# Kernel optimization log

Measured on AMD Instinct MI355X. Metric: run time of the kernel, lower is better.

## Reference

```python
import jax, jax.numpy as jnp
import numpy as np

N = 100000


def _gcn_norm(edge_index, edge_weight, n):
    # PyG gcn_norm: add self loops (weight 1), symmetric normalization.
    src = jnp.concatenate([edge_index[0], jnp.arange(n, dtype=edge_index.dtype)])
    dst = jnp.concatenate([edge_index[1], jnp.arange(n, dtype=edge_index.dtype)])
    ew = jnp.concatenate([edge_weight, jnp.ones((n,), edge_weight.dtype)])
    deg = jax.ops.segment_sum(ew, dst, num_segments=n)  # [N]
    dis = jnp.where(deg > 0, deg ** -0.5, 0.0).astype(edge_weight.dtype)
    norm = dis[src] * ew * dis[dst]  # [E+N]
    return src, dst, norm


def _gcn_conv(x, src, dst, norm, W, b, n):
    h = x @ W                                   # [N, out]
    msg = h[src] * norm[:, None]                # [E+N, out] gather + scale
    out = jax.ops.segment_sum(msg, dst, num_segments=n)  # scatter-add
    return out + b


def setup_inputs() -> dict:
    key = jax.random.key(0)
    ks = jax.random.split(key, 8)
    E = 1600000
    F_in, H, C = 256, 64, 40
    return {
        "x": jax.random.normal(ks[0], (N, F_in), jnp.float32),
        "edge_index": jax.random.randint(ks[1], (2, E), 0, N, jnp.int32),
        "edge_weight": jax.random.uniform(ks[2], (E,), jnp.float32),
        "W0": jax.random.normal(ks[3], (F_in, H), jnp.float32) / np.sqrt(F_in),
        "b0": jnp.zeros((H,), jnp.float32),
        "W1": jax.random.normal(ks[4], (H, H), jnp.float32) / np.sqrt(H),
        "b1": jnp.zeros((H,), jnp.float32),
        "W2": jax.random.normal(ks[5], (H, C), jnp.float32) / np.sqrt(H),
        "b2": jnp.zeros((C,), jnp.float32),
    }


def reference(x, edge_index, edge_weight, W0, b0, W1, b1, W2, b2):
    n = x.shape[0]
    # Edge structure is identical across layers -> compute norm once.
    src, dst, norm = _gcn_norm(edge_index, edge_weight, n)
    # num_layers=3: two hidden GCN layers with relu (dropout = identity in eval)
    h = jax.nn.relu(_gcn_conv(x, src, dst, norm, W0, b0, n))
    h = jax.nn.relu(_gcn_conv(h, src, dst, norm, W1, b1, n))
    h = _gcn_conv(h, src, dst, norm, W2, b2, n)
    return jax.nn.log_softmax(h, axis=1)
```

## Files before the change

### kernel.cpp

```cpp
#include <hip/hip_runtime.h>
#include <math.h>


__device__ __forceinline__ unsigned short f2bf(float f) {
    unsigned u = __float_as_uint(f);
    u += 0x7FFFu + ((u >> 16) & 1u);
    return (unsigned short)(u >> 16);
}
__device__ __forceinline__ float bf2f(unsigned short h) {
    return __uint_as_float(((unsigned)h) << 16);
}

__global__ void k_scan1(const int* __restrict__ cnt, int* __restrict__ excl,
                        int* __restrict__ bsum, int n) {
    __shared__ int sm[256];
    int tid = threadIdx.x;
    int i = blockIdx.x * 256 + tid;
    int v = (i < n) ? cnt[i] : 0;
    sm[tid] = v;
    __syncthreads();
    for (int off = 1; off < 256; off <<= 1) {
        int t = (tid >= off) ? sm[tid - off] : 0;
        __syncthreads();
        sm[tid] += t;
        __syncthreads();
    }
    if (i < n) excl[i] = sm[tid] - v;
    if (tid == 255) bsum[blockIdx.x] = sm[255];
}

__global__ void k_scan2(const int* __restrict__ bsum, int* __restrict__ boff, int nb) {
    __shared__ int sm[512];
    int tid = threadIdx.x;
    int v = (tid < nb) ? bsum[tid] : 0;
    sm[tid] = v;
    __syncthreads();
    for (int off = 1; off < 512; off <<= 1) {
        int t = (tid >= off) ? sm[tid - off] : 0;
        __syncthreads();
        sm[tid] += t;
        __syncthreads();
    }
    boff[tid] = sm[tid] - v;
}

__global__ void k_scan3(int* __restrict__ rowptr, const int* __restrict__ boff,
                        int n, int E) {
    int i = blockIdx.x * blockDim.x + threadIdx.x;
    if (i < n) rowptr[i] += boff[i >> 8];
    if (i == 0) rowptr[n] = E;
}

__global__ void k_place(const int* __restrict__ src, const int* __restrict__ dst,
                        const float* __restrict__ ew, const int* __restrict__ rowptr,
                        const int* __restrict__ pos, unsigned long long* __restrict__ pairP,
                        int E) {
    int e = blockIdx.x * blockDim.x + threadIdx.x;
    if (e < E) {
        int d = dst[e];
        int p = rowptr[d] + pos[e];
        unsigned long long pk = (unsigned long long)__float_as_uint(ew[e]) << 32
                              | (unsigned int)src[e];
        pairP[p] = pk;
    }
}

__global__ void k_deg_dis(const unsigned long long* __restrict__ pairP,
                          const int* __restrict__ rowptr, float* __restrict__ dis, int n) {
    int i = blockIdx.x * blockDim.x + threadIdx.x;
    if (i >= n) return;
    int a = rowptr[i], b = rowptr[i + 1];
    float s = 1.0f;
    for (int p = a; p < b; ++p)
        s += __uint_as_float((unsigned int)(pairP[p] >> 32));
    dis[i] = (s > 0.f) ? rsqrtf(s) : 0.f;
}

__global__ void k_norm_csr(unsigned long long* __restrict__ pairP,
                           const int* __restrict__ rowptr,
                           const float* __restrict__ dis, int n) {
    int i = blockIdx.x * blockDim.x + threadIdx.x;
    if (i >= n) return;
    int a = rowptr[i], b = rowptr[i + 1];
    float dd = dis[i];
    for (int p = a; p < b; ++p) {
        unsigned long long pk = pairP[p];
        int s = (int)(unsigned int)pk;
        float w = __uint_as_float((unsigned int)(pk >> 32));
        float nrm = dis[s] * w * dd;
        pairP[p] = ((unsigned long long)__float_as_uint(nrm) << 32) | (unsigned int)s;
    }
}

template<int K, int NOUT, bool RELU_IN>
__device__ __forceinline__ void gemm_tile_body(
    const float* __restrict__ X, const float* __restrict__ W,
    unsigned short* __restrict__ HB, int nrows, int tile)
{
    constexpr int BM = 64, BN = 64, BK = 32;
    constexpr int T  = K / BK;
    __shared__ float As[BK][BM + 4];
    __shared__ float Bs[BK][BN + 4];

    const int tid = (int)threadIdx.x;
    const int tx  = tid & 15;
    const int ty  = tid >> 4;
    const int r0  = tile * BM;

    const int ar = tid >> 3;
    const int aq = tid & 7;
    const int bk = tid >> 4;
    const int bc = tid & 15;

    const int rowA0 = min(r0 + ar,      nrows - 1);
    const int rowA1 = min(r0 + ar + 32, nrows - 1);
    const float* pA0 = X + (size_t)rowA0 * K + aq * 4;
    const float* pA1 = X + (size_t)rowA1 * K + aq * 4;
    const bool wok = (bc * 4 + 3 < NOUT);
    const float* pB0 = W + (size_t)bk * NOUT + bc * 4;
    const float* pB1 = W + (size_t)(bk + 16) * NOUT + bc * 4;
    const float4 z4 = make_float4(0.f, 0.f, 0.f, 0.f);

    float4 ra0, ra1, rb0, rb1;
    ra0 = *(const float4*)pA0;
    ra1 = *(const float4*)pA1;
    rb0 = wok ? *(const float4*)pB0 : z4;
    rb1 = wok ? *(const float4*)pB1 : z4;

    float acc[4][4] = {};

#pragma unroll 1
    for (int t = 0; t < T; ++t) {
        if (RELU_IN) {
            ra0.x = fmaxf(ra0.x, 0.f); ra0.y = fmaxf(ra0.y, 0.f);
            ra0.z = fmaxf(ra0.z, 0.f); ra0.w = fmaxf(ra0.w, 0.f);
            ra1.x = fmaxf(ra1.x, 0.f); ra1.y = fmaxf(ra1.y, 0.f);
            ra1.z = fmaxf(ra1.z, 0.f); ra1.w = fmaxf(ra1.w, 0.f);
        }
        As[aq * 4 + 0][ar]      = ra0.x;
        As[aq * 4 + 1][ar]      = ra0.y;
        As[aq * 4 + 2][ar]      = ra0.z;
        As[aq * 4 + 3][ar]      = ra0.w;
        As[aq * 4 + 0][ar + 32] = ra1.x;
        As[aq * 4 + 1][ar + 32] = ra1.y;
        As[aq * 4 + 2][ar + 32] = ra1.z;
        As[aq * 4 + 3][ar + 32] = ra1.w;
        *(float4*)&Bs[bk][bc * 4]      = rb0;
        *(float4*)&Bs[bk + 16][bc * 4] = rb1;
        __syncthreads();

        if (t + 1 < T) {
            const int ko = (t + 1) * BK;
            ra0 = *(const float4*)(pA0 + ko);
            ra1 = *(const float4*)(pA1 + ko);
            rb0 = wok ? *(const float4*)(pB0 + (size_t)ko * NOUT) : z4;
            rb1 = wok ? *(const float4*)(pB1 + (size_t)ko * NOUT) : z4;
        }

#pragma unroll
        for (int kk = 0; kk < BK; ++kk) {
            float4 a = *(const float4*)&As[kk][ty * 4];
            float4 b = *(const float4*)&Bs[kk][tx * 4];
            acc[0][0] += a.x * b.x; acc[0][1] += a.x * b.y; acc[0][2] += a.x * b.z; acc[0][3] += a.x * b.w;
            acc[1][0] += a.y * b.x; acc[1][1] += a.y * b.y; acc[1][2] += a.y * b.z; acc[1][3] += a.y * b.w;
            acc[2][0] += a.z * b.x; acc[2][1] += a.z * b.y; acc[2][2] += a.z * b.z; acc[2][3] += a.z * b.w;
            acc[3][0] += a.w * b.x; acc[3][1] += a.w * b.y; acc[3][2] += a.w * b.z; acc[3][3] += a.w * b.w;
        }
        __syncthreads();
    }

    if (tx * 4 + 3 < NOUT) {
#pragma unroll
        for (int i = 0; i < 4; ++i) {
            int row = r0 + ty * 4 + i;
            if (row < nrows) {
                ushort4 hv;
                hv.x = f2bf(acc[i][0]); hv.y = f2bf(acc[i][1]);
                hv.z = f2bf(acc[i][2]); hv.w = f2bf(acc[i][3]);
                *(ushort4*)&HB[(size_t)row * NOUT + tx * 4] = hv;
            }
        }
    }
}

template<int K, int NOUT, bool RELU_IN>
__global__ __launch_bounds__(256) void k_gemm(
    const float* __restrict__ X, const float* __restrict__ W,
    unsigned short* __restrict__ HB, int nrows)
{
    gemm_tile_body<K, NOUT, RELU_IN>(X, W, HB, nrows, (int)blockIdx.x);
}

template<int K, int NOUT, bool RELU_IN>
__global__ __launch_bounds__(256) void k_gemm_cnt(
    const float* __restrict__ X, const float* __restrict__ W,
    unsigned short* __restrict__ HB, int nrows, int ntiles, int ncnt,
    const int* __restrict__ dst, int* __restrict__ cnt, int* __restrict__ pos, int E)
{
    const int b  = (int)blockIdx.x;
    const int m  = min(ntiles, ncnt);
    bool isCnt; int idx;
    if (b < 2 * m) {
        isCnt = ((b & 1) == 0);
        idx   = b >> 1;
    } else {
        int rem = b - 2 * m;
        isCnt = (ncnt > ntiles);
        idx   = m + rem;
    }
    if (!isCnt) {
        gemm_tile_body<K, NOUT, RELU_IN>(X, W, HB, nrows, idx);
    } else {
        int e0     = idx * 256 + (int)threadIdx.x;
        int stride = ncnt * 256;
        for (int e = e0; e < E; e += stride)
            pos[e] = atomicAdd(&cnt[dst[e]], 1);
    }
}

template<int F, bool LSM>
__global__ __launch_bounds__(256) void k_node_agg(
    const unsigned short* __restrict__ hB, const float* __restrict__ dis,
    const float* __restrict__ bias, const int* __restrict__ rowptr,
    const unsigned long long* __restrict__ pairP,
    float* __restrict__ out, int n)
{
    const int lane = threadIdx.x & 63;
    int row = (int)((blockIdx.x * blockDim.x + threadIdx.x) >> 6);
    if (row >= n) return;
    row = __builtin_amdgcn_readfirstlane(row);

    const int a = rowptr[row], b = rowptr[row + 1];
    float d  = dis[row];
    float dd = d * d;
    float sum = 0.f;
    if (lane < F) sum = bf2f(hB[(size_t)row * F + lane]) * dd + bias[lane];

    int j = a;
    for (; j + 4 <= b; j += 4) {
        unsigned long long p0 = pairP[j],     p1 = pairP[j + 1];
        unsigned long long p2 = pairP[j + 2], p3 = pairP[j + 3];
        int   s0 = (int)(unsigned int)p0, s1 = (int)(unsigned int)p1;
        int   s2 = (int)(unsigned int)p2, s3 = (int)(unsigned int)p3;
        float w0 = __uint_as_float((unsigned int)(p0 >> 32));
        float w1 = __uint_as_float((unsigned int)(p1 >> 32));
        float w2 = __uint_as_float((unsigned int)(p2 >> 32));
        float w3 = __uint_as_float((unsigned int)(p3 >> 32));
        if (lane < F) {
            sum += bf2f(hB[(size_t)s0 * F + lane]) * w0;
            sum += bf2f(hB[(size_t)s1 * F + lane]) * w1;
            sum += bf2f(hB[(size_t)s2 * F + lane]) * w2;
            sum += bf2f(hB[(size_t)s3 * F + lane]) * w3;
        }
    }
    for (; j < b; ++j) {
        unsigned long long p = pairP[j];
        int s = (int)(unsigned int)p;
        float w = __uint_as_float((unsigned int)(p >> 32));
        if (lane < F) sum += bf2f(hB[(size_t)s * F + lane]) * w;
    }

    if (LSM) {
        float v = (lane < F) ? sum : -INFINITY;
        float m = v;
#pragma unroll
        for (int off = 32; off; off >>= 1) m = fmaxf(m, __shfl_xor(m, off));
        float e = (lane < F) ? expf(v - m) : 0.f;
        float s2 = e;
#pragma unroll
        for (int off = 32; off; off >>= 1) s2 += __shfl_xor(s2, off);
        float ls = logf(s2);
        if (lane < F) out[(size_t)row * F + lane] = v - m - ls;
    } else {
        if (lane < F) out[(size_t)row * F + lane] = sum;
    }
}

extern "C" void kernel_launch(void* const* d_in, const int* in_sizes, int n_in,
                              void* d_out, int out_size, void* d_ws, size_t ws_size,
                              hipStream_t stream) {
    const float* x  = (const float*)d_in[0];
    const int*   ei = (const int*)  d_in[1];
    const float* ew = (const float*)d_in[2];
    const float* W0 = (const float*)d_in[3];
    const float* b0 = (const float*)d_in[4];
    const float* W1 = (const float*)d_in[5];
    const float* b1 = (const float*)d_in[6];
    const float* W2 = (const float*)d_in[7];
    const float* b2 = (const float*)d_in[8];

    const int E   = in_sizes[2];
    const int H   = in_sizes[4];
    const int Fin = in_sizes[3] / H;
    const int N   = in_sizes[0] / Fin;
    (void)n_in; (void)out_size; (void)ws_size;

    const int* srcv = ei;
    const int* dstv = ei + E;

    float* ws = (float*)d_ws;
    size_t o = 0;
    auto alloc = [&](size_t cnt_) { size_t p = o; o += (cnt_ + 63) & ~(size_t)63; return p; };
    float* dis   = ws + alloc(N);
    float* bufB  = ws + alloc((size_t)N * 64);
    unsigned short* hB = (unsigned short*)(ws + alloc((size_t)N * 32));
    unsigned long long* pairP = (unsigned long long*)(ws + alloc((size_t)E * 2));
    int*   rowptr= (int*)(ws + alloc(N + 1));
    int*   cnt   = (int*)(ws + alloc(N));
    int*   pos   = (int*)(ws + alloc(E));
    int*   bsum  = (int*)(ws + alloc(512));
    int*   boff  = (int*)(ws + alloc(512));
    float* outf  = (float*)d_out;

    const int TB  = 256;
    const int nb1 = (N + 255) / 256;
    const int ntiles = (N + 63) / 64;
    const int XB  = 1024;

    (void)hipMemsetAsync(cnt, 0, (size_t)N * sizeof(int), stream);
    {
        const int m = (ntiles < XB) ? ntiles : XB;
        const int grid = 2 * m + ((ntiles > XB) ? (ntiles - XB) : (XB - ntiles));
        k_gemm_cnt<256, 64, false><<<grid, TB, 0, stream>>>(
            x, W0, hB, N, ntiles, XB, dstv, cnt, pos, E);
    }

    k_scan1<<<nb1, 256, 0, stream>>>(cnt, rowptr, bsum, N);
    k_scan2<<<1, 512, 0, stream>>>(bsum, boff, nb1);
    k_scan3<<<(N + TB - 1) / TB, TB, 0, stream>>>(rowptr, boff, N, E);

    k_place<<<(E + TB - 1) / TB, TB, 0, stream>>>(srcv, dstv, ew, rowptr, pos, pairP, E);

    k_deg_dis <<<(N + TB - 1) / TB, TB, 0, stream>>>(pairP, rowptr, dis, N);
    k_norm_csr<<<(N + TB - 1) / TB, TB, 0, stream>>>(pairP, rowptr, dis, N);

    const int aggGrid = (N * 64 + TB - 1) / TB;

    k_node_agg<64, false><<<aggGrid, TB, 0, stream>>>(hB, dis, b0, rowptr, pairP, bufB, N);

    k_gemm<64, 64, true><<<ntiles, TB, 0, stream>>>(bufB, W1, hB, N);
    k_node_agg<64, false><<<aggGrid, TB, 0, stream>>>(hB, dis, b1, rowptr, pairP, bufB, N);

    k_gemm<64, 40, true><<<ntiles, TB, 0, stream>>>(bufB, W2, hB, N);
    k_node_agg<40, true><<<aggGrid, TB, 0, stream>>>(hB, dis, b2, rowptr, pairP, outf, N);
}
```

Measured before the change: 342.5 us.

## Use wavefront-per-row for degree/norm kernels and stage edge pairs in LDS

The degree and normalization kernels switch from one thread per row to one 64-lane wavefront per row, reading each row's edges with coalesced strided loads and reducing with shuffles. The aggregation kernel now loads up to 64 packed (src, weight) pairs per row cooperatively into shared memory and reads them from LDS, instead of every lane issuing the same global loads. The goal is to cut uncoalesced serial edge walks and redundant global traffic. In exchange, short rows (about 16 edges on average) leave most lanes idle, and the degree sum is added in a different order.

```diff
diff --git a/kernel.cpp b/kernel.cpp
--- a/kernel.cpp
+++ b/kernel.cpp
@@ -65,30 +65,42 @@
     }
 }
 
-__global__ void k_deg_dis(const unsigned long long* __restrict__ pairP,
-                          const int* __restrict__ rowptr, float* __restrict__ dis, int n) {
-    int i = blockIdx.x * blockDim.x + threadIdx.x;
-    if (i >= n) return;
-    int a = rowptr[i], b = rowptr[i + 1];
-    float s = 1.0f;
-    for (int p = a; p < b; ++p)
-        s += __uint_as_float((unsigned int)(pairP[p] >> 32));
-    dis[i] = (s > 0.f) ? rsqrtf(s) : 0.f;
-}
-
-__global__ void k_norm_csr(unsigned long long* __restrict__ pairP,
-                           const int* __restrict__ rowptr,
-                           const float* __restrict__ dis, int n) {
-    int i = blockIdx.x * blockDim.x + threadIdx.x;
-    if (i >= n) return;
-    int a = rowptr[i], b = rowptr[i + 1];
-    float dd = dis[i];
-    for (int p = a; p < b; ++p) {
-        unsigned long long pk = pairP[p];
+__global__ __launch_bounds__(256) void k_deg_dis(
+    const unsigned long long* __restrict__ pairP,
+    const int* __restrict__ rowptr, float* __restrict__ dis, int n)
+{
+    const int lane = threadIdx.x & 63;
+    int row = (int)((blockIdx.x * blockDim.x + threadIdx.x) >> 6);
+    if (row >= n) return;
+    row = __builtin_amdgcn_readfirstlane(row);
+    const int a = rowptr[row], b = rowptr[row + 1];
+    float s = 0.f;
+    for (int idx = a + lane; idx < b; idx += 64)
+        s += __uint_as_float((unsigned int)(pairP[idx] >> 32));
+#pragma unroll
+    for (int off = 32; off; off >>= 1) s += __shfl_xor(s, off);
+    if (lane == 0) {
+        float d = 1.0f + s;
+        dis[row] = (d > 0.f) ? rsqrtf(d) : 0.f;
+    }
+}
+
+__global__ __launch_bounds__(256) void k_norm_csr(
+    unsigned long long* __restrict__ pairP, const int* __restrict__ rowptr,
+    const float* __restrict__ dis, int n)
+{
+    const int lane = threadIdx.x & 63;
+    int row = (int)((blockIdx.x * blockDim.x + threadIdx.x) >> 6);
+    if (row >= n) return;
+    row = __builtin_amdgcn_readfirstlane(row);
+    const int a = rowptr[row], b = rowptr[row + 1];
+    const float dd = dis[row];
+    for (int idx = a + lane; idx < b; idx += 64) {
+        unsigned long long pk = pairP[idx];
         int s = (int)(unsigned int)pk;
         float w = __uint_as_float((unsigned int)(pk >> 32));
         float nrm = dis[s] * w * dd;
-        pairP[p] = ((unsigned long long)__float_as_uint(nrm) << 32) | (unsigned int)s;
+        pairP[idx] = ((unsigned long long)__float_as_uint(nrm) << 32) | (unsigned int)s;
     }
 }
 
@@ -225,7 +237,9 @@
     const unsigned long long* __restrict__ pairP,
     float* __restrict__ out, int n)
 {
+    __shared__ unsigned long long pl[4][64];
     const int lane = threadIdx.x & 63;
+    const int wid  = (threadIdx.x >> 6) & 3;
     int row = (int)((blockIdx.x * blockDim.x + threadIdx.x) >> 6);
     if (row >= n) return;
     row = __builtin_amdgcn_readfirstlane(row);
@@ -236,28 +250,33 @@
     float sum = 0.f;
     if (lane < F) sum = bf2f(hB[(size_t)row * F + lane]) * dd + bias[lane];
 
-    int j = a;
-    for (; j + 4 <= b; j += 4) {
-        unsigned long long p0 = pairP[j],     p1 = pairP[j + 1];
-        unsigned long long p2 = pairP[j + 2], p3 = pairP[j + 3];
-        int   s0 = (int)(unsigned int)p0, s1 = (int)(unsigned int)p1;
-        int   s2 = (int)(unsigned int)p2, s3 = (int)(unsigned int)p3;
-        float w0 = __uint_as_float((unsigned int)(p0 >> 32));
-        float w1 = __uint_as_float((unsigned int)(p1 >> 32));
-        float w2 = __uint_as_float((unsigned int)(p2 >> 32));
-        float w3 = __uint_as_float((unsigned int)(p3 >> 32));
-        if (lane < F) {
-            sum += bf2f(hB[(size_t)s0 * F + lane]) * w0;
-            sum += bf2f(hB[(size_t)s1 * F + lane]) * w1;
-            sum += bf2f(hB[(size_t)s2 * F + lane]) * w2;
-            sum += bf2f(hB[(size_t)s3 * F + lane]) * w3;
-        }
-    }
-    for (; j < b; ++j) {
-        unsigned long long p = pairP[j];
-        int s = (int)(unsigned int)p;
-        float w = __uint_as_float((unsigned int)(p >> 32));
-        if (lane < F) sum += bf2f(hB[(size_t)s * F + lane]) * w;
+    for (int base = a; base < b; base += 64) {
+        int idx = base + lane;
+        pl[wid][lane] = (idx < b) ? pairP[idx] : 0ull;
+        int c = min(64, b - base);
+        int j = 0;
+        for (; j + 4 <= c; j += 4) {
+            unsigned long long p0 = pl[wid][j],     p1 = pl[wid][j + 1];
+            unsigned long long p2 = pl[wid][j + 2], p3 = pl[wid][j + 3];
+            int   s0 = (int)(unsigned int)p0, s1 = (int)(unsigned int)p1;
+            int   s2 = (int)(unsigned int)p2, s3 = (int)(unsigned int)p3;
+            float w0 = __uint_as_float((unsigned int)(p0 >> 32));
+            float w1 = __uint_as_float((unsigned int)(p1 >> 32));
+            float w2 = __uint_as_float((unsigned int)(p2 >> 32));
+            float w3 = __uint_as_float((unsigned int)(p3 >> 32));
+            if (lane < F) {
+                sum += bf2f(hB[(size_t)s0 * F + lane]) * w0;
+                sum += bf2f(hB[(size_t)s1 * F + lane]) * w1;
+                sum += bf2f(hB[(size_t)s2 * F + lane]) * w2;
+                sum += bf2f(hB[(size_t)s3 * F + lane]) * w3;
+            }
+        }
+        for (; j < c; ++j) {
+            unsigned long long p = pl[wid][j];
+            int s = (int)(unsigned int)p;
+            float w = __uint_as_float((unsigned int)(p >> 32));
+            if (lane < F) sum += bf2f(hB[(size_t)s * F + lane]) * w;
+        }
     }
 
     if (LSM) {
@@ -331,10 +350,10 @@
 
     k_place<<<(E + TB - 1) / TB, TB, 0, stream>>>(srcv, dstv, ew, rowptr, pos, pairP, E);
 
-    k_deg_dis <<<(N + TB - 1) / TB, TB, 0, stream>>>(pairP, rowptr, dis, N);
-    k_norm_csr<<<(N + TB - 1) / TB, TB, 0, stream>>>(pairP, rowptr, dis, N);
-
     const int aggGrid = (N * 64 + TB - 1) / TB;
+
+    k_deg_dis <<<aggGrid, TB, 0, stream>>>(pairP, rowptr, dis, N);
+    k_norm_csr<<<aggGrid, TB, 0, stream>>>(pairP, rowptr, dis, N);
 
     k_node_agg<64, false><<<aggGrid, TB, 0, stream>>>(hB, dis, b0, rowptr, pairP, bufB, N);
 
```

After: 331.2 us. -3.3%, faster.
